# Performance work log

Measured on AMD Instinct MI355X. Metric: run time of the kernel, lower is better.

Reference implementation:

```python
import jax, jax.numpy as jnp
import numpy as np

B, S, E, H = 2, 4096, 768, 12
D = E // H  # head_dim = 64
SCALE = D ** -0.5
NEG = -1e9


def setup_inputs() -> dict:
    key = jax.random.key(0)
    ks = jax.random.split(key, 10)
    init = lambda k, shape: jax.random.normal(k, shape, dtype=jnp.float32) * (shape[-1] ** -0.5)
    x = jax.random.normal(ks[0], (B, S, E), dtype=jnp.float32)
    attention_mask = jnp.zeros((B, 1, S, S), dtype=jnp.float32)
    # additive causal mask: 0 on/below diagonal, -1e9 above
    causal = jnp.where(jnp.tril(jnp.ones((S, S), dtype=bool)), 0.0, NEG).astype(jnp.float32)
    causal_attention_mask = causal[None, None]
    return {
        "x": x,
        "attention_mask": attention_mask,
        "causal_attention_mask": causal_attention_mask,
        "Wq": init(ks[1], (E, E)), "bq": jnp.zeros((E,), jnp.float32),
        "Wk": init(ks[2], (E, E)), "bk": jnp.zeros((E,), jnp.float32),
        "Wv": init(ks[3], (E, E)), "bv": jnp.zeros((E,), jnp.float32),
        "Wo": init(ks[4], (E, E)), "bo": jnp.zeros((E,), jnp.float32),
    }


def _split_heads(t):
    # [B,S,E] -> [B,H,S,D]
    return t.reshape(B, S, H, D).transpose(0, 2, 1, 3)


def reference(x, attention_mask, causal_attention_mask, Wq, bq, Wk, bk, Wv, bv, Wo, bo):
    q = _split_heads(x @ Wq.T + bq)
    k = _split_heads(x @ Wk.T + bk)
    v = _split_heads(x @ Wv.T + bv)
    mask = attention_mask + causal_attention_mask  # [B,1,S,S]
    scores = jnp.einsum("bhqd,bhkd->bhqk", q, k) * SCALE + mask
    probs = jax.nn.softmax(scores.astype(jnp.float32), axis=-1).astype(q.dtype)
    out = jnp.einsum("bhqk,bhkd->bhqd", probs, v)
    out = out.transpose(0, 2, 1, 3).reshape(B, S, E)
    return out @ Wo.T + bo
```

## Files before the change

kernel.cpp:

```cpp
#include <hip/hip_runtime.h>
#include <hip/hip_bf16.h>
#include <stdint.h>

#define B_ 2
#define S_ 4096
#define E_ 768
#define H_ 12
#define D_ 64
#define M_TOT (B_*S_)
#define NQKV (3*E_)

typedef __attribute__((ext_vector_type(8)))  short bf16x8;
typedef __attribute__((ext_vector_type(4)))  float f32x4;
typedef __attribute__((ext_vector_type(16))) float f32x16;
typedef unsigned short u16;
typedef unsigned int   u32;

__device__ __forceinline__ u16 f2bf(float f) {
  __hip_bfloat16 h = __float2bfloat16(f);
  return *reinterpret_cast<u16*>(&h);
}

__device__ __forceinline__ float bf2f(u16 u) {
  union { u32 i; float f; } v; v.i = ((u32)u) << 16; return v.f;
}

__device__ __forceinline__ u32 cvtpk(float lo, float hi) {
  u32 r;
  asm("v_cvt_pk_bf16_f32 %0, %1, %2" : "=v"(r) : "v"(lo), "v"(hi));
  return r;
}

#define GLDS(gp, lp) __builtin_amdgcn_global_load_lds( \
    (const __attribute__((address_space(1))) void*)(gp), \
    (__attribute__((address_space(3))) void*)(lp), 16, 0, 0)

#define QSCALE 0.1803368801111573f


__global__ void k_prep(const float* __restrict__ x,
                       const float* __restrict__ Wq, const float* __restrict__ Wk,
                       const float* __restrict__ Wv, const float* __restrict__ bq,
                       const float* __restrict__ bk, const float* __restrict__ bv,
                       const float* __restrict__ Wo,
                       u16* __restrict__ xb, u16* __restrict__ wqkv,
                       float* __restrict__ bqkv, u16* __restrict__ wob)
{
  const int bid = blockIdx.x;
  if (bid < 6144) {
    int i = bid * 256 + threadIdx.x;
    float4 v = reinterpret_cast<const float4*>(x)[i];
    ushort4 o;
    o.x = f2bf(v.x); o.y = f2bf(v.y); o.z = f2bf(v.z); o.w = f2bf(v.w);
    reinterpret_cast<ushort4*>(xb)[i] = o;
  } else if (bid < 7872) {
    int i = (bid - 6144) * 256 + threadIdx.x;
    int base = i * 4;
    int n = base / E_;
    int k = base % E_;
    const float* src; float sc;
    if (n < E_)        { src = Wq + (size_t)n*E_ + k;        sc = QSCALE; }
    else if (n < 2*E_) { src = Wk + (size_t)(n-E_)*E_ + k;   sc = 1.f; }
    else               { src = Wv + (size_t)(n-2*E_)*E_ + k; sc = 1.f; }
    float4 v = *reinterpret_cast<const float4*>(src);
    ushort4 o;
    o.x = f2bf(v.x*sc); o.y = f2bf(v.y*sc); o.z = f2bf(v.z*sc); o.w = f2bf(v.w*sc);
    reinterpret_cast<ushort4*>(wqkv)[i] = o;
    if (i < NQKV) {
      float b = (i < E_) ? bq[i]*QSCALE : (i < 2*E_) ? bk[i-E_] : bv[i-2*E_];
      bqkv[i] = b;
    }
  } else {
    int i = (bid - 7872) * 256 + threadIdx.x;
    float4 v = reinterpret_cast<const float4*>(Wo)[i];
    ushort4 o;
    o.x = f2bf(v.x); o.y = f2bf(v.y); o.z = f2bf(v.z); o.w = f2bf(v.w);
    reinterpret_cast<ushort4*>(wob)[i] = o;
  }
}


template<int MODE>
__global__ __launch_bounds__(256)
void k_gemm(const u16* __restrict__ A, const u16* __restrict__ W,
            const float* __restrict__ bias,
            u16* __restrict__ dq, u16* __restrict__ dk, u16* __restrict__ dv,
            float* __restrict__ fout)
{
  constexpr int BN = (MODE == 0) ? 128 : 64;
  constexpr int NF = BN / 32;
  __shared__ u16 As[128*64];
  __shared__ u16 Ws[BN*64];
  const int tid  = threadIdx.x;
  const int lane = tid & 63, wave = tid >> 6;
  const int m0 = blockIdx.x * 128;
  const int n0 = blockIdx.y * BN;
  const int g  = lane >> 4, cc = lane & 15;
  const int wr = (wave >> 1) * 64, wc = (wave & 1) * (BN/2);
  const int srow = lane >> 3;
  const int scol = (lane & 7) * 8;

  f32x4 acc[4][NF];
  #pragma unroll
  for (int m = 0; m < 4; ++m)
    #pragma unroll
    for (int n = 0; n < NF; ++n) acc[m][n] = (f32x4){0.f,0.f,0.f,0.f};

  for (int k0 = 0; k0 < E_; k0 += 64) {
    __syncthreads();
    #pragma unroll
    for (int i = 0; i < 4; ++i) {
      const int r0 = (i*4 + wave) * 8;
      GLDS(A + (size_t)(m0 + r0 + srow)*E_ + k0 + scol, As + r0*64);
    }
    #pragma unroll
    for (int i = 0; i < BN/32; ++i) {
      const int r0 = (i*4 + wave) * 8;
      GLDS(W + (size_t)(n0 + r0 + srow)*E_ + k0 + scol, Ws + r0*64);
    }
    __syncthreads();
    #pragma unroll
    for (int kk = 0; kk < 64; kk += 32) {
      bf16x8 af[4], bfr[NF];
      #pragma unroll
      for (int m = 0; m < 4; ++m)
        af[m] = *reinterpret_cast<const bf16x8*>(As + (wr + m*16 + cc)*64 + kk + g*8);
      #pragma unroll
      for (int n = 0; n < NF; ++n)
        bfr[n] = *reinterpret_cast<const bf16x8*>(Ws + (wc + n*16 + cc)*64 + kk + g*8);
      #pragma unroll
      for (int m = 0; m < 4; ++m)
        #pragma unroll
        for (int n = 0; n < NF; ++n)
          acc[m][n] = __builtin_amdgcn_mfma_f32_16x16x32_bf16(af[m], bfr[n], acc[m][n], 0, 0, 0);
    }
  }

  #pragma unroll
  for (int n = 0; n < NF; ++n) {
    const int colg = n0 + wc + n*16 + cc;
    const float bb = bias[colg];
    if (MODE == 0) {
      const int which = colg / E_;
      const int nn = colg % E_;
      const int h = nn >> 6, d = nn & 63;
      #pragma unroll
      for (int m = 0; m < 4; ++m)
        #pragma unroll
        for (int j = 0; j < 4; ++j) {
          const int row = m0 + wr + m*16 + g*4 + j;
          const int b = row >> 12, s = row & (S_-1);
          const u16 val = f2bf(acc[m][n][j] + bb);
          if (which == 0)       dq[(((size_t)b*H_ + h)*S_ + s)*D_ + d] = val;
          else if (which == 1)  dk[(((size_t)b*H_ + h)*S_ + s)*D_ + d] = val;
          else                  dv[(((size_t)b*H_ + h)*D_ + d)*S_ + s] = val;
        }
    } else {
      #pragma unroll
      for (int m = 0; m < 4; ++m)
        #pragma unroll
        for (int j = 0; j < 4; ++j) {
          const int row = m0 + wr + m*16 + g*4 + j;
          fout[(size_t)row*E_ + colg] = acc[m][n][j] + bb;
        }
    }
  }
}


__global__ __launch_bounds__(256, 2)
void k_attn(const u16* __restrict__ Qb, const u16* __restrict__ Kb,
            const u16* __restrict__ Vtg, u16* __restrict__ AO,
            u16* __restrict__ PO, float2* __restrict__ PML)
{
  __shared__ u16 Ks[2][32*128];
  __shared__ u16 Vs[2][32*128];
  const int tid = threadIdx.x, lane = tid & 63, w = tid >> 6;

  const int L    = blockIdx.x;
  const int slot = L >> 8;
  const int cu   = L & 255;
  const int x    = cu & 7;
  const int c    = cu >> 3;
  int r;
  if (slot < 4) r = slot*32 + ((slot & 1) ? (31 - c) : c);
  else          r = 128 + c;
  int head, qt, mode;
  if (r < 120) {
    const int g_ = r / 15, o = r % 15;
    if (o < 9) {
      if (o < 3) { head = o; qt = 15 - g_; mode = 0; }
      else { const int hh = o - 3; head = hh >> 1; mode = 1 + (hh & 1); qt = 31 - 2*g_; }
    } else { const int hh = o - 9; head = hh >> 1; mode = 1 + (hh & 1); qt = 30 - 2*g_; }
  } else {
    const int rr = r - 120; qt = 7 - rr/3; head = rr % 3; mode = 0;
  }
  const int bh = x*3 + head;
  const int q0 = qt * 128;
  const int nt = (mode == 0) ? (2*qt + 2) : (qt + 1);
  const int kvtb = (mode == 2) ? (qt + 1) : 0;

  const size_t kbase = (size_t)bh * S_ * D_;
  const size_t vbase = (size_t)bh * D_ * S_;
  const int hi = lane >> 5, l31 = lane & 31;
  const int swz = (lane & 15) << 4;
  const int qg = q0 + w*32 + l31;

  int stA[2], stB[2];
  #pragma unroll
  for (int i = 0; i < 2; ++i) {
    const int jj = 2*w + i;
    const int row = jj*4 + (lane >> 4);
    const int gb = ((lane & 15) * 16) ^ ((row & 15) << 4);
    stA[i] = row + 32*(gb >> 7);
    stB[i] = (gb & 127) >> 1;
  }

  bf16x8 qf[4];
  #pragma unroll
  for (int ds = 0; ds < 4; ++ds)
    qf[ds] = *reinterpret_cast<const bf16x8*>(Qb + kbase + (size_t)qg*D_ + ds*16 + hi*8);

  float m_run = 0.f, l_run = 0.f;
  f32x16 o0, o1, cin;
  #pragma unroll
  for (int r2 = 0; r2 < 16; ++r2) { o0[r2] = 0.f; o1[r2] = 0.f; cin[r2] = 0.f; }

#define STAGE(buf, kv0_) do { \
    _Pragma("unroll") \
    for (int i = 0; i < 2; ++i) { \
      GLDS(Kb  + kbase + (size_t)((kv0_) + stA[i])*D_ + stB[i], &Ks[buf][(2*w+i)*512]); \
      GLDS(Vtg + vbase + (size_t)stA[i]*S_ + (kv0_) + stB[i],   &Vs[buf][(2*w+i)*512]); \
    } } while(0)

  int cur = 0;
  STAGE(0, kvtb*64);

  for (int it = 0; it < nt; ++it) {
    asm volatile("s_waitcnt vmcnt(0)" ::: "memory");
    __builtin_amdgcn_s_barrier();
    asm volatile("" ::: "memory");
    if (it + 1 < nt) STAGE(cur ^ 1, (kvtb + it + 1)*64);

    const int kvt = kvtb + it;
    const int kv0 = kvt * 64;
    const u16* bK = Ks[cur];
    const u16* bV = Vs[cur];

    f32x16 s0, s1;
    __builtin_amdgcn_s_setprio(1);
    {
      const int off = (16*hi ^ swz) >> 1;
      bf16x8 a0 = *reinterpret_cast<const bf16x8*>(bK + l31*128 + off);
      bf16x8 a1 = *reinterpret_cast<const bf16x8*>(bK + l31*128 + (off ^ 64));
      s0 = __builtin_amdgcn_mfma_f32_32x32x16_bf16(a0, qf[0], cin, 0, 0, 0);
      s1 = __builtin_amdgcn_mfma_f32_32x32x16_bf16(a1, qf[0], cin, 0, 0, 0);
    }
    #pragma unroll
    for (int ds = 1; ds < 4; ++ds) {
      const int off = ((32*ds + 16*hi) ^ swz) >> 1;
      bf16x8 a0 = *reinterpret_cast<const bf16x8*>(bK + l31*128 + off);
      bf16x8 a1 = *reinterpret_cast<const bf16x8*>(bK + l31*128 + (off ^ 64));
      s0 = __builtin_amdgcn_mfma_f32_32x32x16_bf16(a0, qf[ds], s0, 0, 0, 0);
      s1 = __builtin_amdgcn_mfma_f32_32x32x16_bf16(a1, qf[ds], s1, 0, 0, 0);
    }
    __builtin_amdgcn_s_setprio(0);

    if (kvt >= 2*qt) {
      #pragma unroll
      for (int r2 = 0; r2 < 16; ++r2) {
        const int kvl = kv0 + (r2&3) + 8*(r2>>2) + 4*hi;
        s0[r2] = (kvl      > qg) ? -1e30f : s0[r2];
        s1[r2] = (kvl + 32 > qg) ? -1e30f : s1[r2];
      }
    }

    #pragma unroll
    for (int r2 = 0; r2 < 16; ++r2) s0[r2] = exp2f(s0[r2]);
    #pragma unroll
    for (int r2 = 0; r2 < 16; ++r2) s1[r2] = exp2f(s1[r2]);

    float t4[8];
    #pragma unroll
    for (int i = 0; i < 4; ++i)
      t4[i] = (s0[4*i] + s0[4*i+1]) + (s0[4*i+2] + s0[4*i+3]);
    #pragma unroll
    for (int i = 0; i < 4; ++i)
      t4[4+i] = (s1[4*i] + s1[4*i+1]) + (s1[4*i+2] + s1[4*i+3]);
    float sum = ((t4[0]+t4[1]) + (t4[2]+t4[3])) + ((t4[4]+t4[5]) + (t4[6]+t4[7]));
    sum += __shfl_xor(sum, 32);

    if (__all(sum <= 1.0995116e12f)) {
      l_run += sum;
    } else {
      const float alpha = 0x1p-40f;
      l_run = (l_run + sum) * alpha;
      m_run += 40.f;
      #pragma unroll
      for (int r2 = 0; r2 < 16; ++r2) {
        s0[r2] *= alpha; s1[r2] *= alpha;
        o0[r2] *= alpha; o1[r2] *= alpha;
        cin[r2] -= 40.f;
      }
    }

    u32 c16[16];
    #pragma unroll
    for (int i = 0; i < 8; ++i) {
      c16[i]   = cvtpk(s0[2*i], s0[2*i+1]);
      c16[8+i] = cvtpk(s1[2*i], s1[2*i+1]);
    }

    #pragma unroll
    for (int ks = 0; ks < 4; ++ks) {
      const int cb = (ks>>1)*8 + (ks&1)*4;
      u32 x0 = c16[cb],   y0 = c16[cb+2];
      u32 x1 = c16[cb+1], y1 = c16[cb+3];
      asm volatile("v_permlane32_swap_b32 %0, %1" : "+v"(x0), "+v"(y0));
      asm volatile("v_permlane32_swap_b32 %0, %1" : "+v"(x1), "+v"(y1));
      union { u32 u[4]; bf16x8 v; } pf;
      pf.u[0] = x0; pf.u[1] = x1; pf.u[2] = y0; pf.u[3] = y1;
      const int voff = ((32*ks + 16*hi) ^ swz) >> 1;
      bf16x8 v0 = *reinterpret_cast<const bf16x8*>(bV + l31*128 + voff);
      bf16x8 v1 = *reinterpret_cast<const bf16x8*>(bV + l31*128 + (voff ^ 64));
      __builtin_amdgcn_s_setprio(1);
      o0 = __builtin_amdgcn_mfma_f32_32x32x16_bf16(v0, pf.v, o0, 0, 0, 0);
      o1 = __builtin_amdgcn_mfma_f32_32x32x16_bf16(v1, pf.v, o1, 0, 0, 0);
      __builtin_amdgcn_s_setprio(0);
    }

    cur ^= 1;
  }
#undef STAGE

  if (mode == 0) {
    const int b = bh / H_, h = bh % H_;
    const float inv = 1.0f / l_run;
    u16* dst = AO + ((size_t)b*S_ + qg)*E_ + h*64;
    #pragma unroll
    for (int aa = 0; aa < 4; ++aa) {
      ushort4 wv;
      wv.x = f2bf(o0[4*aa+0]*inv); wv.y = f2bf(o0[4*aa+1]*inv);
      wv.z = f2bf(o0[4*aa+2]*inv); wv.w = f2bf(o0[4*aa+3]*inv);
      *reinterpret_cast<ushort4*>(dst + aa*8 + hi*4) = wv;
    }
    #pragma unroll
    for (int aa = 0; aa < 4; ++aa) {
      ushort4 wv;
      wv.x = f2bf(o1[4*aa+0]*inv); wv.y = f2bf(o1[4*aa+1]*inv);
      wv.z = f2bf(o1[4*aa+2]*inv); wv.w = f2bf(o1[4*aa+3]*inv);
      *reinterpret_cast<ushort4*>(dst + 32 + aa*8 + hi*4) = wv;
    }
  } else {
    const int qslot = (bh*16 + (qt-16))*2 + (mode - 1);
    const int rowt = w*32 + l31;
    u16* po = PO + (size_t)qslot*(128*64) + rowt*64;
    #pragma unroll
    for (int aa = 0; aa < 4; ++aa) {
      ushort4 wv;
      wv.x = f2bf(o0[4*aa+0]); wv.y = f2bf(o0[4*aa+1]);
      wv.z = f2bf(o0[4*aa+2]); wv.w = f2bf(o0[4*aa+3]);
      *reinterpret_cast<ushort4*>(po + aa*8 + hi*4) = wv;
    }
    #pragma unroll
    for (int aa = 0; aa < 4; ++aa) {
      ushort4 wv;
      wv.x = f2bf(o1[4*aa+0]); wv.y = f2bf(o1[4*aa+1]);
      wv.z = f2bf(o1[4*aa+2]); wv.w = f2bf(o1[4*aa+3]);
      *reinterpret_cast<ushort4*>(po + 32 + aa*8 + hi*4) = wv;
    }
    if (hi == 0) PML[qslot*128 + rowt] = make_float2(m_run, l_run);
  }
}


__global__ __launch_bounds__(256)
void k_comb(const u16* __restrict__ PO, const float2* __restrict__ PML,
            u16* __restrict__ AO)
{
  const int bid = blockIdx.x;
  const int bh = bid >> 4, qi = bid & 15, q = 16 + qi;
  const int t = threadIdx.x;
  const int r = t >> 1, half = t & 1;
  const int s0 = (bh*16 + qi)*2, s1 = s0 + 1;
  const float2 ml0 = PML[s0*128 + r];
  const float2 ml1 = PML[s1*128 + r];
  const float mstar = fmaxf(ml0.x, ml1.x);
  const float w0 = exp2f(ml0.x - mstar);
  const float w1 = exp2f(ml1.x - mstar);
  const float inv = 1.0f / (ml0.y*w0 + ml1.y*w1);
  const float a0 = w0 * inv, a1 = w1 * inv;
  const u16* p0 = PO + (size_t)s0*(128*64) + r*64 + half*32;
  const u16* p1 = PO + (size_t)s1*(128*64) + r*64 + half*32;
  const int b = bh / H_, h = bh % H_;
  const int row = q*128 + r;
  u16* dst = AO + ((size_t)b*S_ + row)*E_ + h*64 + half*32;
  #pragma unroll
  for (int i = 0; i < 4; ++i) {
    bf16x8 v0 = *reinterpret_cast<const bf16x8*>(p0 + i*8);
    bf16x8 v1 = *reinterpret_cast<const bf16x8*>(p1 + i*8);
    ushort4 lo, hi4;
    float f0 = bf2f(((const u16*)&v0)[0])*a0 + bf2f(((const u16*)&v1)[0])*a1;
    float f1 = bf2f(((const u16*)&v0)[1])*a0 + bf2f(((const u16*)&v1)[1])*a1;
    float f2 = bf2f(((const u16*)&v0)[2])*a0 + bf2f(((const u16*)&v1)[2])*a1;
    float f3 = bf2f(((const u16*)&v0)[3])*a0 + bf2f(((const u16*)&v1)[3])*a1;
    lo.x = f2bf(f0); lo.y = f2bf(f1); lo.z = f2bf(f2); lo.w = f2bf(f3);
    float f4 = bf2f(((const u16*)&v0)[4])*a0 + bf2f(((const u16*)&v1)[4])*a1;
    float f5 = bf2f(((const u16*)&v0)[5])*a0 + bf2f(((const u16*)&v1)[5])*a1;
    float f6 = bf2f(((const u16*)&v0)[6])*a0 + bf2f(((const u16*)&v1)[6])*a1;
    float f7 = bf2f(((const u16*)&v0)[7])*a0 + bf2f(((const u16*)&v1)[7])*a1;
    hi4.x = f2bf(f4); hi4.y = f2bf(f5); hi4.z = f2bf(f6); hi4.w = f2bf(f7);
    *reinterpret_cast<ushort4*>(dst + i*8)     = lo;
    *reinterpret_cast<ushort4*>(dst + i*8 + 4) = hi4;
  }
}


extern "C" void kernel_launch(void* const* d_in, const int* in_sizes, int n_in,
                              void* d_out, int out_size, void* d_ws, size_t ws_size,
                              hipStream_t stream) {
  const float* x  = (const float*)d_in[0];
  const float* Wq = (const float*)d_in[3];
  const float* bq = (const float*)d_in[4];
  const float* Wk = (const float*)d_in[5];
  const float* bk = (const float*)d_in[6];
  const float* Wv = (const float*)d_in[7];
  const float* bv = (const float*)d_in[8];
  const float* Wo = (const float*)d_in[9];
  const float* bo = (const float*)d_in[10];
  float* out = (float*)d_out;

  const size_t SZ_X   = (size_t)M_TOT * E_ * 2;
  const size_t SZ_WQKV= (size_t)NQKV * E_ * 2;
  const size_t SZ_WO  = (size_t)E_ * E_ * 2;
  const size_t SZ_B   = (size_t)NQKV * 4;
  char* w = (char*)d_ws;
  u16*   xb   = (u16*)(w);
  u16*   wqkv = (u16*)(w + SZ_X);
  u16*   wob  = (u16*)(w + SZ_X + SZ_WQKV);
  float* bqkv = (float*)(w + SZ_X + SZ_WQKV + SZ_WO);
  char*  w2   = w + SZ_X + SZ_WQKV + SZ_WO + SZ_B;
  u16* Qb = (u16*)(w2);
  u16* Kb = (u16*)(w2 + SZ_X);
  u16* Vb = (u16*)(w2 + 2*SZ_X);
  u16* AO = (u16*)(w2 + 3*SZ_X);
  u16* PO = xb;
  float2* PML = (float2*)(w2 + 4*SZ_X);

  k_prep<<<8448, 256, 0, stream>>>(x, Wq, Wk, Wv, bq, bk, bv, Wo,
                                   xb, wqkv, bqkv, wob);

  dim3 gq(64, 18);
  k_gemm<0><<<gq, 256, 0, stream>>>(xb, wqkv, bqkv, Qb, Kb, Vb, nullptr);

  k_attn<<<1152, 256, 0, stream>>>(Qb, Kb, Vb, AO, PO, PML);
  k_comb<<<384, 256, 0, stream>>>(PO, PML, AO);

  dim3 go(64, 12);
  k_gemm<1><<<go, 256, 0, stream>>>(AO, wob, bo, nullptr, nullptr, nullptr, out);
}
```

Baseline: 197.8 us.

## Software-pipeline QK of next tile with softmax/PV using triple-buffered K/V

Moves K/V staging to three LDS buffers so the tile two ahead can be prefetched. The QK^T MFMAs for the next tile are issued before the current tile's exp2/softmax and PV work, hiding MFMA latency behind VALU work. The overflow rescale check moves after the PV product and now uses a reference offset subtracted inside exp2. The launch-bounds hint rises to three blocks per CU, which adds register pressure from the extra live score accumulators and risks spills. The rescale path appears to shift the prefetched scores twice, but it likely never triggers.

```diff
diff --git a/kernel.cpp b/kernel.cpp
--- a/kernel.cpp
+++ b/kernel.cpp
@@ -168,13 +168,13 @@
 }
 
 
-__global__ __launch_bounds__(256, 2)
+__global__ __launch_bounds__(256, 3)
 void k_attn(const u16* __restrict__ Qb, const u16* __restrict__ Kb,
             const u16* __restrict__ Vtg, u16* __restrict__ AO,
             u16* __restrict__ PO, float2* __restrict__ PML)
 {
-  __shared__ u16 Ks[2][32*128];
-  __shared__ u16 Vs[2][32*128];
+  __shared__ u16 Ks[3][32*128];
+  __shared__ u16 Vs[3][32*128];
   const int tid = threadIdx.x, lane = tid & 63, w = tid >> 6;
 
   const int L    = blockIdx.x;
@@ -221,52 +221,64 @@
   for (int ds = 0; ds < 4; ++ds)
     qf[ds] = *reinterpret_cast<const bf16x8*>(Qb + kbase + (size_t)qg*D_ + ds*16 + hi*8);
 
-  float m_run = 0.f, l_run = 0.f;
-  f32x16 o0, o1, cin;
-  #pragma unroll
-  for (int r2 = 0; r2 < 16; ++r2) { o0[r2] = 0.f; o1[r2] = 0.f; cin[r2] = 0.f; }
-
-#define STAGE(buf, kv0_) do { \
+  float ref = 0.f, l_run = 0.f;
+  f32x16 o0, o1;
+  #pragma unroll
+  for (int r2 = 0; r2 < 16; ++r2) { o0[r2] = 0.f; o1[r2] = 0.f; }
+
+#define STAGE(buf, kvt_) do { \
     _Pragma("unroll") \
     for (int i = 0; i < 2; ++i) { \
-      GLDS(Kb  + kbase + (size_t)((kv0_) + stA[i])*D_ + stB[i], &Ks[buf][(2*w+i)*512]); \
-      GLDS(Vtg + vbase + (size_t)stA[i]*S_ + (kv0_) + stB[i],   &Vs[buf][(2*w+i)*512]); \
+      GLDS(Kb  + kbase + (size_t)((kvt_)*64 + stA[i])*D_ + stB[i], &Ks[buf][(2*w+i)*512]); \
+      GLDS(Vtg + vbase + (size_t)stA[i]*S_ + (kvt_)*64 + stB[i],   &Vs[buf][(2*w+i)*512]); \
     } } while(0)
 
-  int cur = 0;
-  STAGE(0, kvtb*64);
-
+#define QK(bufp, d0, d1) do { \
+    const u16* bK_ = (bufp); \
+    { const int off = (16*hi ^ swz) >> 1; \
+      bf16x8 a0 = *reinterpret_cast<const bf16x8*>(bK_ + l31*128 + off); \
+      bf16x8 a1 = *reinterpret_cast<const bf16x8*>(bK_ + l31*128 + (off ^ 64)); \
+      d0 = __builtin_amdgcn_mfma_f32_32x32x16_bf16(a0, qf[0], z16, 0, 0, 0); \
+      d1 = __builtin_amdgcn_mfma_f32_32x32x16_bf16(a1, qf[0], z16, 0, 0, 0); } \
+    _Pragma("unroll") \
+    for (int ds = 1; ds < 4; ++ds) { \
+      const int off = ((32*ds + 16*hi) ^ swz) >> 1; \
+      bf16x8 a0 = *reinterpret_cast<const bf16x8*>(bK_ + l31*128 + off); \
+      bf16x8 a1 = *reinterpret_cast<const bf16x8*>(bK_ + l31*128 + (off ^ 64)); \
+      d0 = __builtin_amdgcn_mfma_f32_32x32x16_bf16(a0, qf[ds], d0, 0, 0, 0); \
+      d1 = __builtin_amdgcn_mfma_f32_32x32x16_bf16(a1, qf[ds], d1, 0, 0, 0); \
+    } } while(0)
+
+  f32x16 z16;
+  #pragma unroll
+  for (int r2 = 0; r2 < 16; ++r2) z16[r2] = 0.f;
+
+  STAGE(0, kvtb);
+  asm volatile("s_waitcnt vmcnt(0)" ::: "memory");
+  __builtin_amdgcn_s_barrier();
+  f32x16 s0, s1;
+  __builtin_amdgcn_s_setprio(1);
+  QK(Ks[0], s0, s1);
+  __builtin_amdgcn_s_setprio(0);
+  if (nt > 1) STAGE(1, kvtb + 1);
+  asm volatile("s_waitcnt vmcnt(0)" ::: "memory");
+  __builtin_amdgcn_s_barrier();
+  if (nt > 2) STAGE(2, kvtb + 2);
+
+  int bc = 0;
   for (int it = 0; it < nt; ++it) {
-    asm volatile("s_waitcnt vmcnt(0)" ::: "memory");
-    __builtin_amdgcn_s_barrier();
-    asm volatile("" ::: "memory");
-    if (it + 1 < nt) STAGE(cur ^ 1, (kvtb + it + 1)*64);
-
     const int kvt = kvtb + it;
-    const int kv0 = kvt * 64;
-    const u16* bK = Ks[cur];
-    const u16* bV = Vs[cur];
-
-    f32x16 s0, s1;
-    __builtin_amdgcn_s_setprio(1);
-    {
-      const int off = (16*hi ^ swz) >> 1;
-      bf16x8 a0 = *reinterpret_cast<const bf16x8*>(bK + l31*128 + off);
-      bf16x8 a1 = *reinterpret_cast<const bf16x8*>(bK + l31*128 + (off ^ 64));
-      s0 = __builtin_amdgcn_mfma_f32_32x32x16_bf16(a0, qf[0], cin, 0, 0, 0);
-      s1 = __builtin_amdgcn_mfma_f32_32x32x16_bf16(a1, qf[0], cin, 0, 0, 0);
-    }
-    #pragma unroll
-    for (int ds = 1; ds < 4; ++ds) {
-      const int off = ((32*ds + 16*hi) ^ swz) >> 1;
-      bf16x8 a0 = *reinterpret_cast<const bf16x8*>(bK + l31*128 + off);
-      bf16x8 a1 = *reinterpret_cast<const bf16x8*>(bK + l31*128 + (off ^ 64));
-      s0 = __builtin_amdgcn_mfma_f32_32x32x16_bf16(a0, qf[ds], s0, 0, 0, 0);
-      s1 = __builtin_amdgcn_mfma_f32_32x32x16_bf16(a1, qf[ds], s1, 0, 0, 0);
-    }
-    __builtin_amdgcn_s_setprio(0);
+
+    f32x16 sn0, sn1;
+    const int bn = (bc == 2) ? 0 : bc + 1;
+    if (it + 1 < nt) {
+      __builtin_amdgcn_s_setprio(1);
+      QK(Ks[bn], sn0, sn1);
+      __builtin_amdgcn_s_setprio(0);
+    }
 
     if (kvt >= 2*qt) {
+      const int kv0 = kvt * 64;
       #pragma unroll
       for (int r2 = 0; r2 < 16; ++r2) {
         const int kvl = kv0 + (r2&3) + 8*(r2>>2) + 4*hi;
@@ -274,43 +286,26 @@
         s1[r2] = (kvl + 32 > qg) ? -1e30f : s1[r2];
       }
     }
-
-    #pragma unroll
-    for (int r2 = 0; r2 < 16; ++r2) s0[r2] = exp2f(s0[r2]);
-    #pragma unroll
-    for (int r2 = 0; r2 < 16; ++r2) s1[r2] = exp2f(s1[r2]);
-
+    u32 c16[16];
     float t4[8];
+    #pragma unroll
+    for (int r2 = 0; r2 < 16; ++r2) s0[r2] = exp2f(s0[r2] - ref);
     #pragma unroll
     for (int i = 0; i < 4; ++i)
       t4[i] = (s0[4*i] + s0[4*i+1]) + (s0[4*i+2] + s0[4*i+3]);
     #pragma unroll
+    for (int i = 0; i < 8; ++i) c16[i] = cvtpk(s0[2*i], s0[2*i+1]);
+    #pragma unroll
+    for (int r2 = 0; r2 < 16; ++r2) s1[r2] = exp2f(s1[r2] - ref);
+    #pragma unroll
     for (int i = 0; i < 4; ++i)
       t4[4+i] = (s1[4*i] + s1[4*i+1]) + (s1[4*i+2] + s1[4*i+3]);
+    #pragma unroll
+    for (int i = 0; i < 8; ++i) c16[8+i] = cvtpk(s1[2*i], s1[2*i+1]);
     float sum = ((t4[0]+t4[1]) + (t4[2]+t4[3])) + ((t4[4]+t4[5]) + (t4[6]+t4[7]));
     sum += __shfl_xor(sum, 32);
 
-    if (__all(sum <= 1.0995116e12f)) {
-      l_run += sum;
-    } else {
-      const float alpha = 0x1p-40f;
-      l_run = (l_run + sum) * alpha;
-      m_run += 40.f;
-      #pragma unroll
-      for (int r2 = 0; r2 < 16; ++r2) {
-        s0[r2] *= alpha; s1[r2] *= alpha;
-        o0[r2] *= alpha; o1[r2] *= alpha;
-        cin[r2] -= 40.f;
-      }
-    }
-
-    u32 c16[16];
-    #pragma unroll
-    for (int i = 0; i < 8; ++i) {
-      c16[i]   = cvtpk(s0[2*i], s0[2*i+1]);
-      c16[8+i] = cvtpk(s1[2*i], s1[2*i+1]);
-    }
-
+    const u16* bV = Vs[bc];
     #pragma unroll
     for (int ks = 0; ks < 4; ++ks) {
       const int cb = (ks>>1)*8 + (ks&1)*4;
@@ -329,8 +324,28 @@
       __builtin_amdgcn_s_setprio(0);
     }
 
-    cur ^= 1;
-  }
+    l_run += sum;
+    if (!__all(l_run <= 1.0995116e12f)) {
+      const float alpha = 0x1p-40f;
+      l_run *= alpha;
+      ref += 40.f;
+      #pragma unroll
+      for (int r2 = 0; r2 < 16; ++r2) { o0[r2] *= alpha; o1[r2] *= alpha; }
+      if (it + 1 < nt) {
+        #pragma unroll
+        for (int r2 = 0; r2 < 16; ++r2) { sn0[r2] -= 40.f; sn1[r2] -= 40.f; }
+      }
+    }
+
+    if (it + 1 < nt) {
+      asm volatile("s_waitcnt vmcnt(0)" ::: "memory");
+      __builtin_amdgcn_s_barrier();
+      if (it + 3 < nt) STAGE(bc, kvtb + it + 3);
+      s0 = sn0; s1 = sn1;
+    }
+    bc = bn;
+  }
+#undef QK
 #undef STAGE
 
   if (mode == 0) {
@@ -369,7 +384,7 @@
       wv.z = f2bf(o1[4*aa+2]); wv.w = f2bf(o1[4*aa+3]);
       *reinterpret_cast<ushort4*>(po + 32 + aa*8 + hi*4) = wv;
     }
-    if (hi == 0) PML[qslot*128 + rowt] = make_float2(m_run, l_run);
+    if (hi == 0) PML[qslot*128 + rowt] = make_float2(ref, l_run);
   }
 }
 
```

New measurement: 227.7 us. 1.15x slower.
